# Performance work log

Measured on AMD Instinct MI355X. Metric: run time of the kernel, lower is better.

Reference implementation:

```python
import jax, jax.numpy as jnp
import numpy as np

B, S, D_IN, H = 4, 2048, 1024, 1024


def setup_inputs() -> dict:
    key = jax.random.key(0)
    k1, k2, k3 = jax.random.split(key, 3)
    qkv = jax.random.normal(k1, (B, S, D_IN), dtype=jnp.float32)
    # True = position is masked out (torch masked_fill semantics)
    attention_mask = jax.random.randint(k2, (B, S), 0, 2).astype(jnp.bool_)
    W_qkv = jax.random.normal(k3, (D_IN, 3 * H), dtype=jnp.float32) * (1.0 / np.sqrt(D_IN))
    b_qkv = jnp.zeros((3 * H,), dtype=jnp.float32)
    return {"qkv": qkv, "attention_mask": attention_mask, "W_qkv": W_qkv, "b_qkv": b_qkv}


def reference(qkv, attention_mask, W_qkv, b_qkv):
    # fused QKV projection: (B, S, 3H)
    proj = jnp.einsum("bsd,dh->bsh", qkv, W_qkv) + b_qkv
    q, k, v = jnp.split(proj, 3, axis=-1)  # each (B, S, H)
    scaling_factor = jnp.asarray(H, dtype=q.dtype) ** 0.5
    q = q * scaling_factor  # NOTE: original multiplies (not divides) by sqrt(H)
    scores = jnp.einsum("bqh,bkh->bqk", q, k)  # (B, S, S)
    # mask broadcasts over the query dim: masked keys get -inf
    neg_inf = jnp.asarray(-jnp.inf, dtype=scores.dtype)
    scores = jnp.where(attention_mask[:, None, :], neg_inf, scores)
    distributions = jax.nn.softmax(scores, axis=-1)  # dropout p=0.0 -> identity
    return jnp.einsum("bqk,bkh->bqh", distributions, v)
```

## Files before the change

### kernel.cpp

```cpp
#include <hip/hip_runtime.h>
#include <stdint.h>


#define S_LEN 2048
#define BATCH 4
#define DIN   1024
#define HDIM  1024
#define N3H   3072
#define NTOK  8192

typedef unsigned short u16;
typedef __attribute__((ext_vector_type(8))) short bf16x8;
typedef __attribute__((ext_vector_type(4))) float f32x4;
typedef __attribute__((ext_vector_type(16))) float f32x16;
typedef __attribute__((ext_vector_type(4))) unsigned short u16x4;

__device__ __forceinline__ u16 f2bf(float x) {
  union { float f; unsigned u; } c; c.f = x;
  unsigned r = c.u + 0x7fffu + ((c.u >> 16) & 1u);
  return (u16)(r >> 16);
}
__device__ __forceinline__ float bf2f(u16 h) {
  union { unsigned u; float f; } c; c.u = ((unsigned)h) << 16;
  return c.f;
}

__device__ __forceinline__ void gload16(const void* g, void* lds) {
  auto* gp = reinterpret_cast<const __attribute__((address_space(1))) void*>(
      reinterpret_cast<uintptr_t>(g));
  auto* lp = reinterpret_cast<__attribute__((address_space(3))) void*>(
      (unsigned)reinterpret_cast<uintptr_t>(lds));
  __builtin_amdgcn_global_load_lds(gp, lp, 16, 0, 0);
}

__device__ __forceinline__ void stage_tile(const u16* __restrict__ g, int ld,
                                           u16* lds, int wave, int lane) {
  const int rlane = lane >> 3;
  const int kb    = (lane & 7) ^ (rlane & 7);
#pragma unroll
  for (int h = 0; h < 4; ++h) {
    const int instr = wave * 4 + h;
    const u16* gp = g + (size_t)(instr * 8 + rlane) * ld + kb * 8;
    gload16(gp, (char*)lds + instr * 1024);
  }
}

__device__ __forceinline__ void stage_half8(const u16* __restrict__ g, int ld,
                                            u16* lds, int wave, int lane) {
  const int rlane = lane >> 3;
  const int kb    = (lane & 7) ^ (rlane & 7);
#pragma unroll
  for (int h = 0; h < 2; ++h) {
    const int instr = wave * 2 + h;
    const u16* gp = g + (size_t)(instr * 8 + rlane) * ld + kb * 8;
    gload16(gp, (char*)lds + instr * 1024);
  }
}

__device__ __forceinline__ void stage_tile8(
    const u16* __restrict__ A, const u16* __restrict__ B, int lda, int ldb,
    u16* ldsbuf, int wave, int lane) {
  stage_half8(A, lda, ldsbuf, wave, lane);
  stage_half8(A + (size_t)128 * lda, lda, ldsbuf + 8192, wave, lane);
  stage_half8(B, ldb, ldsbuf + 16384, wave, lane);
  stage_half8(B + (size_t)128 * ldb, ldb, ldsbuf + 24576, wave, lane);
}

__device__ __forceinline__ bf16x8 frag32(const u16* t, int wq, int sub, int kh,
                                         int lane) {
  const int r5   = lane & 31;
  const int row  = wq * 64 + sub * 32 + r5;
  const int slot = (kh * 2 + (lane >> 5)) ^ (r5 & 7);
  return *(const bf16x8*)(t + row * 64 + slot * 8);
}

__device__ __forceinline__ bf16x8 dsr128(int addr) {
  bf16x8 r;
  asm volatile("ds_read_b128 %0, %1" : "=v"(r) : "v"(addr));
  return r;
}

__device__ __forceinline__ f32x16 mfma32(bf16x8 a, bf16x8 b, f32x16 c) {
  return __builtin_amdgcn_mfma_f32_32x32x16_bf16(a, b, c, 0, 0, 0);
}

__device__ __forceinline__ const u16* selA(const u16* Ah, const u16* Al, int t) {
  return (t < 32) ? Ah : Al;
}
__device__ __forceinline__ const u16* selB(const u16* Bh, const u16* Bl, int t) {
  return ((t >> 4) == 1) ? Bl : Bh;
}

template <int MODE, int BUF>
__device__ __forceinline__ void tileK(
    int t, u16* lds, f32x16 acc[4][2],
    const u16* __restrict__ Ah, const u16* __restrict__ Al,
    const u16* __restrict__ Bh, const u16* __restrict__ Bl,
    int lda, int ldb, const int (&vA)[2][4], const int (&vB)[2][4],
    int wave, int lane)
{
  bf16x8 fb0[4], fb1[4], fa[2][4];

#pragma unroll
  for (int kh = 0; kh < 4; ++kh) {
    fb0[kh]   = dsr128(vB[BUF][kh]);
    fb1[kh]   = dsr128(vB[BUF][kh] + 4096);
    fa[0][kh] = dsr128(vA[BUF][kh]);
    fa[1][kh] = dsr128(vA[BUF][kh] + 4096);
  }
  asm volatile("s_waitcnt lgkmcnt(0)" ::: "memory");
  __builtin_amdgcn_sched_barrier(0);
  __builtin_amdgcn_s_setprio(1);
#pragma unroll
  for (int kh = 0; kh < 4; ++kh) {
    acc[0][0] = mfma32(fa[0][kh], fb0[kh], acc[0][0]);
    acc[1][0] = mfma32(fa[1][kh], fb0[kh], acc[1][0]);
    acc[0][1] = mfma32(fa[0][kh], fb1[kh], acc[0][1]);
    acc[1][1] = mfma32(fa[1][kh], fb1[kh], acc[1][1]);
  }
  __builtin_amdgcn_s_setprio(0);

#pragma unroll
  for (int kh = 0; kh < 4; ++kh) {
    fa[0][kh] = dsr128(vA[BUF][kh] + 8192);
    fa[1][kh] = dsr128(vA[BUF][kh] + 12288);
  }
  asm volatile("s_waitcnt lgkmcnt(0)" ::: "memory");
  __builtin_amdgcn_sched_barrier(0);
  __builtin_amdgcn_s_setprio(1);
#pragma unroll
  for (int kh = 0; kh < 4; ++kh) {
    acc[2][0] = mfma32(fa[0][kh], fb0[kh], acc[2][0]);
    acc[3][0] = mfma32(fa[1][kh], fb0[kh], acc[3][0]);
    acc[2][1] = mfma32(fa[0][kh], fb1[kh], acc[2][1]);
    acc[3][1] = mfma32(fa[1][kh], fb1[kh], acc[3][1]);
  }
  __builtin_amdgcn_s_setprio(0);

  __builtin_amdgcn_s_barrier();
  if (MODE == 2) {
    stage_tile8(selA(Ah, Al, t + 2) + ((t + 2) & 15) * 64,
                selB(Bh, Bl, t + 2) + ((t + 2) & 15) * 64,
                lda, ldb, lds + BUF * 32768, wave, lane);
    asm volatile("s_waitcnt vmcnt(8)" ::: "memory");
  }
  if (MODE == 1) asm volatile("s_waitcnt vmcnt(0)" ::: "memory");
  __builtin_amdgcn_s_barrier();
}

__device__ __forceinline__ void gemm256_split3(
    const u16* __restrict__ Ah, const u16* __restrict__ Al,
    const u16* __restrict__ Bh, const u16* __restrict__ Bl,
    int lda, int ldb, f32x16 acc[4][2], u16* lds,
    int wm, int wn, int wave, int lane)
{
#pragma unroll
  for (int a = 0; a < 4; ++a)
#pragma unroll
    for (int b = 0; b < 2; ++b)
#pragma unroll
      for (int r = 0; r < 16; ++r) acc[a][b][r] = 0.f;

  const int r5 = lane & 31, hi = lane >> 5, x = r5 & 7;
  const int vb = r5 * 128 + ((x ^ hi) << 4);
  const int LB = (int)(unsigned)(uintptr_t)(void*)lds;
  int vA[2][4], vB[2][4];
#pragma unroll
  for (int b = 0; b < 2; ++b)
#pragma unroll
    for (int kh = 0; kh < 4; ++kh) {
      const int vk = vb ^ (kh << 5);
      vA[b][kh] = LB + b * 65536 + wm * 16384 + vk;
      vB[b][kh] = LB + b * 65536 + 32768 + wn * 8192 + vk;
    }

  stage_tile8(Ah, Bh, lda, ldb, lds, wave, lane);
  stage_tile8(Ah + 64, Bh + 64, lda, ldb, lds + 32768, wave, lane);
  asm volatile("s_waitcnt vmcnt(8)" ::: "memory");
  __builtin_amdgcn_s_barrier();

#pragma unroll 1
  for (int t = 0; t < 46; t += 2) {
    tileK<2, 0>(t,     lds, acc, Ah, Al, Bh, Bl, lda, ldb, vA, vB, wave, lane);
    tileK<2, 1>(t + 1, lds, acc, Ah, Al, Bh, Bl, lda, ldb, vA, vB, wave, lane);
  }
  tileK<1, 0>(46, lds, acc, Ah, Al, Bh, Bl, lda, ldb, vA, vB, wave, lane);
  tileK<0, 1>(47, lds, acc, Ah, Al, Bh, Bl, lda, ldb, vA, vB, wave, lane);
}

__device__ __forceinline__ void gemm_core_plain(
    const u16* __restrict__ A, const u16* __restrict__ B,
    int lda, int ldb, int K, f32x16 acc[2][2])
{
  __shared__ __align__(16) u16 lds[2 * 8192];
  u16* aT = lds; u16* bT = lds + 8192;
  const int tid  = threadIdx.x;
  const int wave = tid >> 6, lane = tid & 63;
  const int wm = wave >> 1, wn = wave & 1;

#pragma unroll
  for (int i = 0; i < 2; ++i)
#pragma unroll
    for (int j = 0; j < 2; ++j)
#pragma unroll
      for (int r = 0; r < 16; ++r) acc[i][j][r] = 0.f;

  for (int k0 = 0; k0 < K; k0 += 64) {
    stage_tile(A + k0, lda, aT, wave, lane);
    stage_tile(B + k0, ldb, bT, wave, lane);
    __syncthreads();
#pragma unroll
    for (int kh = 0; kh < 4; ++kh) {
      bf16x8 fa[2];
#pragma unroll
      for (int i = 0; i < 2; ++i) fa[i] = frag32(aT, wm, i, kh, lane);
#pragma unroll
      for (int j = 0; j < 2; ++j) {
        const bf16x8 fb = frag32(bT, wn, j, kh, lane);
#pragma unroll
        for (int i = 0; i < 2; ++i)
          acc[i][j] = __builtin_amdgcn_mfma_f32_32x32x16_bf16(fa[i], fb, acc[i][j], 0, 0, 0);
      }
    }
    __syncthreads();
  }
}

#define ROW32(r, lane) (((r) & 3) + 8 * ((r) >> 2) + 4 * ((lane) >> 5))

__global__ void prep_mask_kernel(const unsigned char* __restrict__ m,
                                 float* __restrict__ bias) {
  __shared__ int isBool;
  if (threadIdx.x == 0) isBool = 0;
  __syncthreads();
  for (int i = threadIdx.x; i < NTOK; i += 256)
    if ((i & 3) && m[i]) isBool = 1;
  __syncthreads();
  const int stride = isBool ? 1 : 4;
  const float ninf = -__builtin_inff();
  for (int i = threadIdx.x; i < NTOK; i += 256)
    bias[i] = m[(size_t)i * stride] ? ninf : 0.f;
}

__global__ __launch_bounds__(256) void split_f32_kernel(
    const float* __restrict__ x, u16* __restrict__ hi, u16* __restrict__ lo) {
  const int i = (blockIdx.x * 256 + threadIdx.x) * 4;
  const f32x4 v = *(const f32x4*)(x + i);
  u16x4 h, l;
#pragma unroll
  for (int c = 0; c < 4; ++c) {
    h[c] = f2bf(v[c]);
    l[c] = f2bf(v[c] - bf2f(h[c]));
  }
  *(u16x4*)(hi + i) = h;
  *(u16x4*)(lo + i) = l;
}

__global__ __launch_bounds__(256) void splitWT_kernel(
    const float* __restrict__ W, u16* __restrict__ whi, u16* __restrict__ wlo) {
  __shared__ float tile[32][33];
  const int t = threadIdx.x;
  const int n0 = blockIdx.x * 32;
  const int d0 = blockIdx.y * 32;
  const int dr = t >> 3, nc = (t & 7) * 4;
  const f32x4 v = *(const f32x4*)(W + (size_t)(d0 + dr) * N3H + n0 + nc);
#pragma unroll
  for (int c = 0; c < 4; ++c) tile[dr][nc + c] = v[c];
  __syncthreads();
  const int nr = t >> 3, dc = (t & 7) * 4;
  u16x4 h, l;
#pragma unroll
  for (int c = 0; c < 4; ++c) {
    const float x = tile[dc + c][nr];
    h[c] = f2bf(x);
    l[c] = f2bf(x - bf2f(h[c]));
  }
  const size_t o = (size_t)(n0 + nr) * DIN + d0 + dc;
  *(u16x4*)(whi + o) = h;
  *(u16x4*)(wlo + o) = l;
}

__global__ __launch_bounds__(512, 2) void proj_qk256_kernel(
    const u16* __restrict__ Ahi, const u16* __restrict__ Alo,
    const u16* __restrict__ Whi, const u16* __restrict__ Wlo,
    const float* __restrict__ bias,
    u16* __restrict__ qhi, u16* __restrict__ qlo,
    u16* __restrict__ khi, u16* __restrict__ klo)
{
  __shared__ __align__(16) u16 lds[2 * 4 * 8192];
  const int bx = blockIdx.x, by = blockIdx.y;
  const int tid = threadIdx.x, wave = tid >> 6, lane = tid & 63;
  const int wm = wave >> 2, wn = wave & 3;

  f32x16 acc[4][2];
  gemm256_split3(Ahi + (size_t)by * 256 * DIN, Alo + (size_t)by * 256 * DIN,
                 Whi + (size_t)bx * 256 * DIN, Wlo + (size_t)bx * 256 * DIN,
                 DIN, DIN, acc, lds, wm, wn, wave, lane);

#pragma unroll
  for (int a = 0; a < 4; ++a) {
#pragma unroll
    for (int b = 0; b < 2; ++b) {
#pragma unroll
      for (int r = 0; r < 16; ++r) {
        const int row = by * 256 + wm * 128 + a * 32 + ROW32(r, lane);
        const int col = bx * 256 + wn * 64 + b * 32 + (lane & 31);
        const float v = acc[a][b][r] + bias[col];
        const u16 h = f2bf(v);
        const u16 l = f2bf(v - bf2f(h));
        if (col < HDIM) {
          const size_t idx = (size_t)row * HDIM + col;
          qhi[idx] = h; qlo[idx] = l;
        } else {
          const size_t idx = (size_t)row * HDIM + (col - HDIM);
          khi[idx] = h; klo[idx] = l;
        }
      }
    }
  }
}

__global__ __launch_bounds__(256, 2) void proj_v_kernel(
    const u16* __restrict__ Ahi, const u16* __restrict__ Whi,
    const float* __restrict__ bias, u16* __restrict__ vt)
{
  const int bx = blockIdx.x, by = blockIdx.y;
  f32x16 acc[2][2];
  gemm_core_plain(Ahi + (size_t)by * 128 * DIN,
                  Whi + (size_t)(2048 + bx * 128) * DIN,
                  DIN, DIN, DIN, acc);
  const int lane = threadIdx.x & 63, wave = threadIdx.x >> 6;
  const int wm = wave >> 1, wn = wave & 1;
#pragma unroll
  for (int i = 0; i < 2; ++i) {
#pragma unroll
    for (int j = 0; j < 2; ++j) {
#pragma unroll
      for (int r = 0; r < 16; ++r) {
        const int row = by * 128 + wm * 64 + i * 32 + ROW32(r, lane);
        const int b = row >> 11, s = row & 2047;
        const int hcol = bx * 128 + wn * 64 + j * 32 + (lane & 31);
        const float v = acc[i][j][r] + bias[2 * HDIM + hcol];
        vt[((size_t)b * HDIM + hcol) * S_LEN + s] = f2bf(v);
      }
    }
  }
}

__global__ __launch_bounds__(512, 2) void scores256_kernel(
    const u16* __restrict__ qhi, const u16* __restrict__ qlo,
    const u16* __restrict__ khi, const u16* __restrict__ klo,
    const float* __restrict__ maskbias, float* __restrict__ scores)
{
  __shared__ __align__(16) u16 lds[2 * 4 * 8192];
  const int id = blockIdx.x;
  const int b  = id >> 6;
  const int by = (id >> 3) & 7;
  const int bx = id & 7;
  const int tid = threadIdx.x, wave = tid >> 6, lane = tid & 63;
  const int wm = wave >> 2, wn = wave & 3;

  f32x16 acc[4][2];
  const size_t qoff = ((size_t)b * S_LEN + by * 256) * HDIM;
  const size_t koff = ((size_t)b * S_LEN + bx * 256) * HDIM;
  gemm256_split3(qhi + qoff, qlo + qoff, khi + koff, klo + koff,
                 HDIM, HDIM, acc, lds, wm, wn, wave, lane);

#pragma unroll
  for (int a = 0; a < 4; ++a) {
#pragma unroll
    for (int bj = 0; bj < 2; ++bj) {
#pragma unroll
      for (int r = 0; r < 16; ++r) {
        const int q   = by * 256 + wm * 128 + a * 32 + ROW32(r, lane);
        const int key = bx * 256 + wn * 64 + bj * 32 + (lane & 31);
        scores[((size_t)b * S_LEN + q) * S_LEN + key] =
            32.0f * acc[a][bj][r] + maskbias[b * S_LEN + key];
      }
    }
  }
}

__global__ __launch_bounds__(256) void softmax_kernel(float* __restrict__ scores) {
  const int wave = threadIdx.x >> 6, lane = threadIdx.x & 63;
  const int row = blockIdx.x * 4 + wave;
  float* srow = scores + (size_t)row * S_LEN;

  f32x4 v[8];
#pragma unroll
  for (int c = 0; c < 8; ++c) v[c] = ((const f32x4*)srow)[c * 64 + lane];

  float m = -__builtin_inff();
#pragma unroll
  for (int c = 0; c < 8; ++c)
    m = fmaxf(m, fmaxf(fmaxf(v[c][0], v[c][1]), fmaxf(v[c][2], v[c][3])));
#pragma unroll
  for (int o = 32; o > 0; o >>= 1) m = fmaxf(m, __shfl_xor(m, o));

  float s = 0.f;
#pragma unroll
  for (int c = 0; c < 8; ++c) {
#pragma unroll
    for (int e = 0; e < 4; ++e) {
      v[c][e] = __expf(v[c][e] - m);
      s += v[c][e];
    }
  }
#pragma unroll
  for (int o = 32; o > 0; o >>= 1) s += __shfl_xor(s, o);
  const float inv = 1.0f / s;

  u16* prow = (u16*)srow;
#pragma unroll
  for (int c = 0; c < 8; ++c) {
    u16x4 o4 = { f2bf(v[c][0] * inv), f2bf(v[c][1] * inv),
                 f2bf(v[c][2] * inv), f2bf(v[c][3] * inv) };
    ((u16x4*)prow)[c * 64 + lane] = o4;
  }
}

__global__ __launch_bounds__(256, 2) void pv_kernel(
    const u16* __restrict__ P, const u16* __restrict__ vt, float* __restrict__ out)
{
  const int id   = blockIdx.x;
  const int xcd  = id & 7;
  const int s    = id >> 3;
  const int b    = s >> 4;
  const int slot = s & 15;
  const int bx   = (xcd & 1) * 4 + (slot & 3);
  const int by   = (xcd >> 1) * 4 + (slot >> 2);

  f32x16 acc[2][2];
  gemm_core_plain(P + ((size_t)b * S_LEN + by * 128) * (2 * S_LEN),
                  vt + ((size_t)b * HDIM + bx * 128) * S_LEN,
                  2 * S_LEN, S_LEN, S_LEN, acc);
  const int lane = threadIdx.x & 63, wave = threadIdx.x >> 6;
  const int wm = wave >> 1, wn = wave & 1;
#pragma unroll
  for (int i = 0; i < 2; ++i) {
#pragma unroll
    for (int j = 0; j < 2; ++j) {
#pragma unroll
      for (int r = 0; r < 16; ++r) {
        const int q = by * 128 + wm * 64 + i * 32 + ROW32(r, lane);
        const int h = bx * 128 + wn * 64 + j * 32 + (lane & 31);
        out[((size_t)b * S_LEN + q) * HDIM + h] = acc[i][j][r];
      }
    }
  }
}

extern "C" void kernel_launch(void* const* d_in, const int* in_sizes, int n_in,
                              void* d_out, int out_size, void* d_ws, size_t ws_size,
                              hipStream_t stream)
{
  const float* qkv  = (const float*)d_in[0];
  const void*  mask = d_in[1];
  const float* W    = (const float*)d_in[2];
  const float* bias = (const float*)d_in[3];
  float* out = (float*)d_out;
  char* ws = (char*)d_ws;

  const size_t off_mask = 0;
  const size_t off_Whi  = 32768;
  const size_t off_Wlo  = off_Whi + (size_t)N3H * DIN * 2;
  const size_t off_Qhi  = off_Wlo + (size_t)N3H * DIN * 2;
  const size_t off_Qlo  = off_Qhi + (size_t)NTOK * HDIM * 2;
  const size_t off_Khi  = off_Qlo + (size_t)NTOK * HDIM * 2;
  const size_t off_Klo  = off_Khi + (size_t)NTOK * HDIM * 2;
  const size_t off_Vt   = off_Klo + (size_t)NTOK * HDIM * 2;
  const size_t off_A    = off_Vt + (size_t)NTOK * HDIM * 2;
  const size_t off_Alo  = off_A + (size_t)NTOK * DIN * 2;
  const size_t off_sc   = off_A;

  float* maskbias = (float*)(ws + off_mask);
  u16* Whi = (u16*)(ws + off_Whi);  u16* Wlo = (u16*)(ws + off_Wlo);
  u16* Qhi = (u16*)(ws + off_Qhi);  u16* Qlo = (u16*)(ws + off_Qlo);
  u16* Khi = (u16*)(ws + off_Khi);  u16* Klo = (u16*)(ws + off_Klo);
  u16* Vt  = (u16*)(ws + off_Vt);
  u16* Ahi = (u16*)(ws + off_A);    u16* Alo = (u16*)(ws + off_Alo);
  float* scores = (float*)(ws + off_sc);

  prep_mask_kernel<<<1, 256, 0, stream>>>((const unsigned char*)mask, maskbias);
  split_f32_kernel<<<NTOK * DIN / 1024, 256, 0, stream>>>(qkv, Ahi, Alo);
  splitWT_kernel<<<dim3(N3H / 32, DIN / 32), 256, 0, stream>>>(W, Whi, Wlo);
  proj_qk256_kernel<<<dim3(2 * HDIM / 256, NTOK / 256), 512, 0, stream>>>(
      Ahi, Alo, Whi, Wlo, bias, Qhi, Qlo, Khi, Klo);
  proj_v_kernel<<<dim3(HDIM / 128, NTOK / 128, 1), 256, 0, stream>>>(
      Ahi, Whi, bias, Vt);
  scores256_kernel<<<64 * BATCH, 512, 0, stream>>>(
      Qhi, Qlo, Khi, Klo, maskbias, scores);
  softmax_kernel<<<NTOK / 4, 256, 0, stream>>>(scores);
  pv_kernel<<<8 * 16 * BATCH, 256, 0, stream>>>(
      (const u16*)scores, Vt, out);
}
```

Baseline: 410.7 us.

## Fuse split-bf16 hi/lo products per K-slice instead of three sequential K passes

```diff
diff --git a/kernel.cpp b/kernel.cpp
--- a/kernel.cpp
+++ b/kernel.cpp
@@ -45,27 +45,6 @@
   }
 }
 
-__device__ __forceinline__ void stage_half8(const u16* __restrict__ g, int ld,
-                                            u16* lds, int wave, int lane) {
-  const int rlane = lane >> 3;
-  const int kb    = (lane & 7) ^ (rlane & 7);
-#pragma unroll
-  for (int h = 0; h < 2; ++h) {
-    const int instr = wave * 2 + h;
-    const u16* gp = g + (size_t)(instr * 8 + rlane) * ld + kb * 8;
-    gload16(gp, (char*)lds + instr * 1024);
-  }
-}
-
-__device__ __forceinline__ void stage_tile8(
-    const u16* __restrict__ A, const u16* __restrict__ B, int lda, int ldb,
-    u16* ldsbuf, int wave, int lane) {
-  stage_half8(A, lda, ldsbuf, wave, lane);
-  stage_half8(A + (size_t)128 * lda, lda, ldsbuf + 8192, wave, lane);
-  stage_half8(B, ldb, ldsbuf + 16384, wave, lane);
-  stage_half8(B + (size_t)128 * ldb, ldb, ldsbuf + 24576, wave, lane);
-}
-
 __device__ __forceinline__ bf16x8 frag32(const u16* t, int wq, int sub, int kh,
                                          int lane) {
   const int r5   = lane & 31;
@@ -74,6 +53,28 @@
   return *(const bf16x8*)(t + row * 64 + slot * 8);
 }
 
+__device__ __forceinline__ void stage32(const u16* __restrict__ g, int ld,
+                                        u16* lds, int wave, int lane) {
+  const int rlane = lane >> 2;
+  const int kb    = (lane & 3) ^ (rlane & 3);
+#pragma unroll
+  for (int h = 0; h < 2; ++h) {
+    const int instr = wave * 2 + h;
+    const u16* gp = g + (size_t)(instr * 16 + rlane) * ld + kb * 8;
+    gload16(gp, (char*)lds + instr * 1024);
+  }
+}
+
+__device__ __forceinline__ void stage_set(
+    const u16* __restrict__ Ah, const u16* __restrict__ Al,
+    const u16* __restrict__ Bh, const u16* __restrict__ Bl,
+    int koff, int lda, int ldb, u16* buf, int wave, int lane) {
+  stage32(Ah + koff, lda, buf,         wave, lane);
+  stage32(Al + koff, lda, buf + 8192,  wave, lane);
+  stage32(Bh + koff, ldb, buf + 16384, wave, lane);
+  stage32(Bl + koff, ldb, buf + 24576, wave, lane);
+}
+
 __device__ __forceinline__ bf16x8 dsr128(int addr) {
   bf16x8 r;
   asm volatile("ds_read_b128 %0, %1" : "=v"(r) : "v"(addr));
@@ -84,64 +85,45 @@
   return __builtin_amdgcn_mfma_f32_32x32x16_bf16(a, b, c, 0, 0, 0);
 }
 
-__device__ __forceinline__ const u16* selA(const u16* Ah, const u16* Al, int t) {
-  return (t < 32) ? Ah : Al;
-}
-__device__ __forceinline__ const u16* selB(const u16* Bh, const u16* Bl, int t) {
-  return ((t >> 4) == 1) ? Bl : Bh;
-}
-
 template <int MODE, int BUF>
-__device__ __forceinline__ void tileK(
+__device__ __forceinline__ void tileF(
     int t, u16* lds, f32x16 acc[4][2],
     const u16* __restrict__ Ah, const u16* __restrict__ Al,
     const u16* __restrict__ Bh, const u16* __restrict__ Bl,
-    int lda, int ldb, const int (&vA)[2][4], const int (&vB)[2][4],
+    int lda, int ldb, const int (&vA)[2][2], const int (&vB)[2][2],
     int wave, int lane)
 {
-  bf16x8 fb0[4], fb1[4], fa[2][4];
-
-#pragma unroll
-  for (int kh = 0; kh < 4; ++kh) {
-    fb0[kh]   = dsr128(vB[BUF][kh]);
-    fb1[kh]   = dsr128(vB[BUF][kh] + 4096);
-    fa[0][kh] = dsr128(vA[BUF][kh]);
-    fa[1][kh] = dsr128(vA[BUF][kh] + 4096);
-  }
-  asm volatile("s_waitcnt lgkmcnt(0)" ::: "memory");
-  __builtin_amdgcn_sched_barrier(0);
-  __builtin_amdgcn_s_setprio(1);
-#pragma unroll
-  for (int kh = 0; kh < 4; ++kh) {
-    acc[0][0] = mfma32(fa[0][kh], fb0[kh], acc[0][0]);
-    acc[1][0] = mfma32(fa[1][kh], fb0[kh], acc[1][0]);
-    acc[0][1] = mfma32(fa[0][kh], fb1[kh], acc[0][1]);
-    acc[1][1] = mfma32(fa[1][kh], fb1[kh], acc[1][1]);
-  }
-  __builtin_amdgcn_s_setprio(0);
-
-#pragma unroll
-  for (int kh = 0; kh < 4; ++kh) {
-    fa[0][kh] = dsr128(vA[BUF][kh] + 8192);
-    fa[1][kh] = dsr128(vA[BUF][kh] + 12288);
-  }
-  asm volatile("s_waitcnt lgkmcnt(0)" ::: "memory");
-  __builtin_amdgcn_sched_barrier(0);
-  __builtin_amdgcn_s_setprio(1);
-#pragma unroll
-  for (int kh = 0; kh < 4; ++kh) {
-    acc[2][0] = mfma32(fa[0][kh], fb0[kh], acc[2][0]);
-    acc[3][0] = mfma32(fa[1][kh], fb0[kh], acc[3][0]);
-    acc[2][1] = mfma32(fa[0][kh], fb1[kh], acc[2][1]);
-    acc[3][1] = mfma32(fa[1][kh], fb1[kh], acc[3][1]);
-  }
-  __builtin_amdgcn_s_setprio(0);
-
+#pragma unroll
+  for (int kh = 0; kh < 2; ++kh) {
+    bf16x8 fah[4], fal[4], fbh[2], fbl[2];
+#pragma unroll
+    for (int s = 0; s < 4; ++s) {
+      fah[s] = dsr128(vA[BUF][kh] + s * 2048);
+      fal[s] = dsr128(vA[BUF][kh] + 16384 + s * 2048);
+    }
+#pragma unroll
+    for (int j = 0; j < 2; ++j) {
+      fbh[j] = dsr128(vB[BUF][kh] + j * 2048);
+      fbl[j] = dsr128(vB[BUF][kh] + 16384 + j * 2048);
+    }
+    asm volatile("s_waitcnt lgkmcnt(0)" ::: "memory");
+    __builtin_amdgcn_sched_barrier(0);
+    __builtin_amdgcn_s_setprio(1);
+#pragma unroll
+    for (int s = 0; s < 4; ++s) {
+#pragma unroll
+      for (int j = 0; j < 2; ++j) {
+        acc[s][j] = mfma32(fah[s], fbh[j], acc[s][j]);
+        acc[s][j] = mfma32(fah[s], fbl[j], acc[s][j]);
+        acc[s][j] = mfma32(fal[s], fbh[j], acc[s][j]);
+      }
+    }
+    __builtin_amdgcn_s_setprio(0);
+  }
   __builtin_amdgcn_s_barrier();
   if (MODE == 2) {
-    stage_tile8(selA(Ah, Al, t + 2) + ((t + 2) & 15) * 64,
-                selB(Bh, Bl, t + 2) + ((t + 2) & 15) * 64,
-                lda, ldb, lds + BUF * 32768, wave, lane);
+    stage_set(Ah, Al, Bh, Bl, (t + 2) * 32, lda, ldb,
+              lds + BUF * 32768, wave, lane);
     asm volatile("s_waitcnt vmcnt(8)" ::: "memory");
   }
   if (MODE == 1) asm volatile("s_waitcnt vmcnt(0)" ::: "memory");
@@ -161,31 +143,31 @@
 #pragma unroll
       for (int r = 0; r < 16; ++r) acc[a][b][r] = 0.f;
 
-  const int r5 = lane & 31, hi = lane >> 5, x = r5 & 7;
-  const int vb = r5 * 128 + ((x ^ hi) << 4);
+  const int r5 = lane & 31, hi = lane >> 5;
   const int LB = (int)(unsigned)(uintptr_t)(void*)lds;
-  int vA[2][4], vB[2][4];
+  int vA[2][2], vB[2][2];
 #pragma unroll
   for (int b = 0; b < 2; ++b)
 #pragma unroll
-    for (int kh = 0; kh < 4; ++kh) {
-      const int vk = vb ^ (kh << 5);
-      vA[b][kh] = LB + b * 65536 + wm * 16384 + vk;
-      vB[b][kh] = LB + b * 65536 + 32768 + wn * 8192 + vk;
-    }
-
-  stage_tile8(Ah, Bh, lda, ldb, lds, wave, lane);
-  stage_tile8(Ah + 64, Bh + 64, lda, ldb, lds + 32768, wave, lane);
+    for (int kh = 0; kh < 2; ++kh) {
+      const int slot = (((kh << 1) ^ hi ^ (r5 & 3)) << 4);
+      const int vb = r5 * 64 + slot;
+      vA[b][kh] = LB + b * 65536 + wm * 8192 + vb;
+      vB[b][kh] = LB + b * 65536 + 32768 + wn * 4096 + vb;
+    }
+
+  stage_set(Ah, Al, Bh, Bl, 0,  lda, ldb, lds,         wave, lane);
+  stage_set(Ah, Al, Bh, Bl, 32, lda, ldb, lds + 32768, wave, lane);
   asm volatile("s_waitcnt vmcnt(8)" ::: "memory");
   __builtin_amdgcn_s_barrier();
 
 #pragma unroll 1
-  for (int t = 0; t < 46; t += 2) {
-    tileK<2, 0>(t,     lds, acc, Ah, Al, Bh, Bl, lda, ldb, vA, vB, wave, lane);
-    tileK<2, 1>(t + 1, lds, acc, Ah, Al, Bh, Bl, lda, ldb, vA, vB, wave, lane);
-  }
-  tileK<1, 0>(46, lds, acc, Ah, Al, Bh, Bl, lda, ldb, vA, vB, wave, lane);
-  tileK<0, 1>(47, lds, acc, Ah, Al, Bh, Bl, lda, ldb, vA, vB, wave, lane);
+  for (int t = 0; t < 30; t += 2) {
+    tileF<2, 0>(t,     lds, acc, Ah, Al, Bh, Bl, lda, ldb, vA, vB, wave, lane);
+    tileF<2, 1>(t + 1, lds, acc, Ah, Al, Bh, Bl, lda, ldb, vA, vB, wave, lane);
+  }
+  tileF<1, 0>(30, lds, acc, Ah, Al, Bh, Bl, lda, ldb, vA, vB, wave, lane);
+  tileF<0, 1>(31, lds, acc, Ah, Al, Bh, Bl, lda, ldb, vA, vB, wave, lane);
 }
 
 __device__ __forceinline__ void gemm_core_plain(
@@ -287,7 +269,7 @@
     u16* __restrict__ qhi, u16* __restrict__ qlo,
     u16* __restrict__ khi, u16* __restrict__ klo)
 {
-  __shared__ __align__(16) u16 lds[2 * 4 * 8192];
+  __shared__ __align__(128) u16 lds[2 * 4 * 8192];
   const int bx = blockIdx.x, by = blockIdx.y;
   const int tid = threadIdx.x, wave = tid >> 6, lane = tid & 63;
   const int wm = wave >> 2, wn = wave & 3;
@@ -352,7 +334,7 @@
     const u16* __restrict__ khi, const u16* __restrict__ klo,
     const float* __restrict__ maskbias, float* __restrict__ scores)
 {
-  __shared__ __align__(16) u16 lds[2 * 4 * 8192];
+  __shared__ __align__(128) u16 lds[2 * 4 * 8192];
   const int id = blockIdx.x;
   const int b  = id >> 6;
   const int by = (id >> 3) & 7;
```

After: 426.0 us. 1.04x slower.
